# Kernel tuning notes

Measured on AMD Instinct MI355X. Metric: run time of the kernel, lower is better.

The kernel has to match this reference:

```python
import jax, jax.numpy as jnp
import numpy as np

B, N, T, F = 256, 64, 50, 2
E, H, R = 64, 128, 30


def setup_inputs() -> dict:
    key = jax.random.key(0)
    ks = jax.random.split(key, 16)
    rn = lambda k, shp, s=0.1: jax.random.normal(k, shp, jnp.float32) * s
    return {
        "src": jax.random.normal(ks[0], (B, N, T, F), jnp.float32),
        "trg": jax.random.normal(ks[1], (B, R, F), jnp.float32),
        # spatial encoder: residual Linear (no bias) + GCNConv weight/bias
        "W_res": rn(ks[2], (F, E)),
        "W_gcn": rn(ks[3], (F, E)),
        "b_gcn": jnp.zeros((E,), jnp.float32),
        # encoder LSTMCell (PyTorch gate order i,f,g,o); b = b_ih + b_hh fused
        "W_ih_e": rn(ks[4], (E, 4 * H)),
        "W_hh_e": rn(ks[5], (H, 4 * H)),
        "b_e": jnp.zeros((4 * H,), jnp.float32),
        # decoder: linear1 (2->E), LSTMCell (E->H), linear2 (H->2)
        "W1": rn(ks[6], (F, E)),
        "b1": jnp.zeros((E,), jnp.float32),
        "W_ih_d": rn(ks[7], (E, 4 * H)),
        "W_hh_d": rn(ks[8], (H, 4 * H)),
        "b_d": jnp.zeros((4 * H,), jnp.float32),
        "W2": rn(ks[9], (H, F)),
        "b2": jnp.zeros((F,), jnp.float32),
    }


def _lstm_step(h, c, xt, W_ih, W_hh, b):
    g = xt @ W_ih + h @ W_hh + b
    i, f, gg, o = jnp.split(g, 4, axis=-1)
    c = jax.nn.sigmoid(f) * c + jax.nn.sigmoid(i) * jnp.tanh(gg)
    h = jax.nn.sigmoid(o) * jnp.tanh(c)
    return h, c


def _forward(src, trg, W_res, W_gcn, b_gcn, W_ih_e, W_hh_e, b_e,
             W1, b1, W_ih_d, W_hh_d, b_d, W2, b2):
    # ---- EncoderSpatial: distance-weighted GCNConv over per-(sample,t) full graph ----
    x = jnp.swapaxes(src, 1, 2)                       # [B,T,N,F]
    diff = x[:, :, :, None, :] - x[:, :, None, :, :]  # [B,T,N,N,F]
    dist = jnp.linalg.norm(diff, axis=-1)             # [B,T,N,N]
    dist = jnp.where(dist == 0.0, 1e-6, dist)
    w = jnp.minimum(1.0 / dist, 1.0)                  # clipped inverse distance
    eye = jnp.eye(N, dtype=x.dtype)
    w = w * (1.0 - eye) + eye                         # remove self loops, GCN adds them with weight 1
    dinv = jnp.sum(w, axis=-1) ** -0.5                # [B,T,N]
    A = w * dinv[..., :, None] * dinv[..., None, :]   # sym-normalized adjacency
    gcn = jnp.einsum('btij,btjf->btif', A, x @ W_gcn) + b_gcn
    enc = jax.nn.relu(gcn + x @ W_res)                # [B,T,N,E]
    emb = enc[:, :, 0, :]                             # target-agent embeddings [B,T,E]
    inputs0 = x[:, :, 0, :]                           # target-agent positions  [B,T,F]

    # ---- LSTM encoder over T steps ----
    def enc_step(carry, xt):
        h, c = _lstm_step(carry[0], carry[1], xt, W_ih_e, W_hh_e, b_e)
        return (h, c), None
    h0 = jnp.zeros((B, H), src.dtype)
    (h, c), _ = jax.lax.scan(enc_step, (h0, h0), jnp.swapaxes(emb, 0, 1))

    def dec_step(carry, _):
        xin, h, c = carry
        ed = jax.nn.relu(xin @ W1 + b1)
        h, c = _lstm_step(h, c, ed, W_ih_d, W_hh_d, b_d)
        out = h @ W2 + b2
        return (out, h, c), out
    (_, _, _), outs = jax.lax.scan(dec_step, (inputs0[:, -1, :], h, c), None, length=R)
    return jnp.swapaxes(outs, 0, 1)                   # reg: [B,R,F]


def reference(src, trg, W_res, W_gcn, b_gcn, W_ih_e, W_hh_e, b_e,
              W1, b1, W_ih_d, W_hh_d, b_d, W2, b2):
    return _forward(src, trg, W_res, W_gcn, b_gcn, W_ih_e, W_hh_e, b_e,
                    W1, b1, W_ih_d, W_hh_d, b_d, W2, b2)
```

## Files before the change

### kernel.cpp

```cpp
#include <hip/hip_runtime.h>

#define Bn 256
#define Nn 64
#define Tn 50
#define Fn 2
#define En 64
#define Hn 128
#define Rn 30
#define G4 512

typedef _Float16 h2    __attribute__((ext_vector_type(2)));
typedef _Float16 f16x8 __attribute__((ext_vector_type(8)));
typedef float    f32x4 __attribute__((ext_vector_type(4)));

__device__ __forceinline__ float sigf(float x) {
    return __builtin_amdgcn_rcpf(1.0f + __expf(-x));
}
__device__ __forceinline__ float tanh_fast(float x) {
    return 1.0f - 2.0f * __builtin_amdgcn_rcpf(__expf(2.0f * x) + 1.0f);
}
__device__ __forceinline__ float dot2(h2 a, h2 b, float c) {
#if __has_builtin(__builtin_amdgcn_fdot2)
    return __builtin_amdgcn_fdot2(a, b, c, false);
#else
    return fmaf((float)a[0], (float)b[0], fmaf((float)a[1], (float)b[1], c));
#endif
}
__device__ __forceinline__ h2 pack2(float a, float b) {
    h2 r; r[0] = (_Float16)a; r[1] = (_Float16)b; return r;
}
__device__ __forceinline__ h2 bch2(float u)        { return __builtin_bit_cast(h2, u); }
__device__ __forceinline__ h2 bchu(unsigned int u) { return __builtin_bit_cast(h2, u); }

__device__ __forceinline__ void blockbar() {
    __builtin_amdgcn_sched_barrier(0);
    asm volatile("s_waitcnt lgkmcnt(0)" ::: "memory");
    __builtin_amdgcn_s_barrier();
    __builtin_amdgcn_sched_barrier(0);
}

__global__ __launch_bounds__(512) void k_pre(const float* __restrict__ src,
                                             const float* __restrict__ W_res,
                                             const float* __restrict__ W_gcn,
                                             const float* __restrict__ b_gcn,
                                             const float* __restrict__ W_ih_e,
                                             const float* __restrict__ b_e,
                                             _Float16* __restrict__ XI)
{
    const int tid  = threadIdx.x;
    const int lane = tid & 63;
    const int wv   = tid >> 6;
    const int task0 = blockIdx.x * 16;

    __shared__ __align__(16) _Float16 elds[16][64];
    __shared__ float2 xs[8][Nn];

    const float wg0 = W_gcn[lane], wg1 = W_gcn[En + lane];
    const float wr0 = W_res[lane], wr1 = W_res[En + lane];
    const float bg  = b_gcn[lane];

    #pragma unroll
    for (int it = 0; it < 2; it++) {
        const int task = task0 + (wv << 1) + it;
        const int b = task / Tn;
        const int t = task - b * Tn;

        const float2 xv = *reinterpret_cast<const float2*>(
            src + (((size_t)b * Nn + lane) * Tn + t) * Fn);
        const float x0 = xv.x, x1 = xv.y;
        xs[wv][lane] = xv;

        float rowsum = 0.0f, w0 = 0.0f;
        #pragma unroll
        for (int k = 0; k < Nn; k++) {
            const float2 o = xs[wv][k];
            const float dx = x0 - o.x, dy = x1 - o.y;
            const float w = fminf(__builtin_amdgcn_rsqf(dx * dx + dy * dy), 1.0f);
            rowsum += w;
            if (k == 0) w0 = w;
        }
        const float dinv  = __builtin_amdgcn_rsqf(rowsum);
        const float dinv0 = __shfl(dinv, 0);
        const float a = w0 * dinv0 * dinv;

        float p0 = a * x0, p1 = a * x1;
        #pragma unroll
        for (int off = 32; off; off >>= 1) {
            p0 += __shfl_xor(p0, off);
            p1 += __shfl_xor(p1, off);
        }
        const float xa = __shfl(x0, 0);
        const float xb = __shfl(x1, 0);

        const float v = p0 * wg0 + p1 * wg1 + bg + xa * wr0 + xb * wr1;
        elds[(wv << 1) + it][lane] = (_Float16)fmaxf(v, 0.0f);
    }

    const int colp = (tid & 3) * 128 + (tid >> 2);
    h2 wih[32];
    #pragma unroll
    for (int q = 0; q < 32; q++)
        wih[q] = pack2(W_ih_e[(size_t)(2 * q) * G4 + colp],
                       W_ih_e[(size_t)(2 * q + 1) * G4 + colp]);
    const float be = b_e[colp];
    __syncthreads();

    #pragma unroll
    for (int it = 0; it < 16; it++) {
        const float4* e4 = reinterpret_cast<const float4*>(&elds[it][0]);
        float acc = be;
        #pragma unroll
        for (int q = 0; q < 8; q++) {
            const float4 u = e4[q];
            acc = dot2(wih[4 * q + 0], bch2(u.x), acc);
            acc = dot2(wih[4 * q + 1], bch2(u.y), acc);
            acc = dot2(wih[4 * q + 2], bch2(u.z), acc);
            acc = dot2(wih[4 * q + 3], bch2(u.w), acc);
        }
        XI[(size_t)(task0 + it) * G4 + tid] = (_Float16)acc;
    }
}

__global__ __launch_bounds__(512) void k_seq(
    const _Float16* __restrict__ XI,
    const float* __restrict__ src,
    const float* __restrict__ W_hh_e,
    const float* __restrict__ W1,     const float* __restrict__ b1,
    const float* __restrict__ W_ih_d, const float* __restrict__ W_hh_d,
    const float* __restrict__ b_d,
    const float* __restrict__ W2,     const float* __restrict__ b2,
    float* __restrict__ out)
{
    const int tid  = threadIdx.x;
    const int lane = tid & 63;
    const int wv   = tid >> 6;
    const int l15  = lane & 15;
    const int lg   = lane >> 4;
    const int cc   = wv * 16 + l15;
    const int bq0  = blockIdx.x * 4;

    __shared__ __align__(16) _Float16 hbuf[2][576];
    __shared__ __align__(16) _Float16 wi_frag[8 * 8 * 64 * 8];
    __shared__ __align__(16) float    redw[2][8][4][2];

    f16x8 bfr[4][4];
    #pragma unroll
    for (int g = 0; g < 4; g++)
        #pragma unroll
        for (int kt = 0; kt < 4; kt++) {
            f16x8 v;
            #pragma unroll
            for (int j = 0; j < 8; j++)
                v[j] = (_Float16)W_hh_e[(size_t)(kt * 32 + lg * 8 + j) * G4 + g * 128 + cc];
            bfr[g][kt] = v;
        }

    if (tid < 288) reinterpret_cast<float*>(&hbuf[0][0])[tid] = 0.0f;

    float cst = 0.0f;
    char* const hb0 = reinterpret_cast<char*>(&hbuf[0][0]);
    char* const hb1 = reinterpret_cast<char*>(&hbuf[1][0]);
    const _Float16* const XIrow = XI + (size_t)(bq0 + lg) * Tn * G4 + cc * 4;

    uint2 xi0, xi1;
    xi0 = *reinterpret_cast<const uint2*>(XIrow + 0 * G4);
    xi1 = *reinterpret_cast<const uint2*>(XIrow + 1 * G4);
    __syncthreads();

    for (int t = 0; t < Tn; t += 2) {
        uint2 nxt0, nxt1;
        const int t2 = (t + 2 < Tn) ? t + 2 : t;
        const int t3 = (t + 3 < Tn) ? t + 3 : t;
        nxt0 = *reinterpret_cast<const uint2*>(XIrow + (size_t)t2 * G4);
        nxt1 = *reinterpret_cast<const uint2*>(XIrow + (size_t)t3 * G4);

        #pragma unroll
        for (int half = 0; half < 2; half++) {
            char* const hr = half ? hb1 : hb0;
            char* const hw = half ? hb0 : hb1;
            const uint2 xiv = half ? xi1 : xi0;

            f16x8 af[4];
            #pragma unroll
            for (int kt = 0; kt < 4; kt++)
                af[kt] = *reinterpret_cast<const f16x8*>(
                    hr + (l15 & 3) * 288 + kt * 64 + lg * 16);

            f32x4 acc[4] = {};
            #pragma unroll
            for (int kt = 0; kt < 4; kt++)
                #pragma unroll
                for (int g = 0; g < 4; g++)
                    acc[g] = __builtin_amdgcn_mfma_f32_16x16x32_f16(af[kt], bfr[g][kt], acc[g], 0, 0, 0);

            float ga[4];
            #pragma unroll
            for (int g = 0; g < 4; g++) {
                const float s01 = (lg & 1) ? acc[g][1] : acc[g][0];
                const float s23 = (lg & 1) ? acc[g][3] : acc[g][2];
                ga[g] = (lg & 2) ? s23 : s01;
            }

            const h2 lo = bchu(xiv.x);
            const h2 hi = bchu(xiv.y);
            const float gi = ga[0] + (float)lo[0];
            const float gf = ga[1] + (float)lo[1];
            const float gg = ga[2] + (float)hi[0];
            const float go = ga[3] + (float)hi[1];
            cst = sigf(gf) * cst + sigf(gi) * tanh_fast(gg);
            const float hv = sigf(go) * tanh_fast(cst);

            *reinterpret_cast<_Float16*>(hw + lg * 288 + cc * 2) = (_Float16)hv;
            blockbar();
        }
        xi0 = nxt0; xi1 = nxt1;
    }

    #pragma unroll
    for (int g = 0; g < 4; g++)
        #pragma unroll
        for (int kt = 0; kt < 4; kt++) {
            f16x8 v;
            #pragma unroll
            for (int j = 0; j < 8; j++)
                v[j] = (_Float16)W_hh_d[(size_t)(kt * 32 + lg * 8 + j) * G4 + g * 128 + cc];
            bfr[g][kt] = v;
        }
    #pragma unroll
    for (int g = 0; g < 4; g++)
        #pragma unroll
        for (int kt2 = 0; kt2 < 2; kt2++) {
            f16x8 v;
            #pragma unroll
            for (int j = 0; j < 8; j++)
                v[j] = (_Float16)W_ih_d[(size_t)(kt2 * 32 + lg * 8 + j) * G4 + g * 128 + cc];
            *reinterpret_cast<f16x8*>(&wi_frag[((wv * 8 + g * 2 + kt2) * 64 + lane) * 8]) = v;
        }

    const float bd0 = b_d[cc], bd1 = b_d[128 + cc], bd2 = b_d[256 + cc], bd3 = b_d[384 + cc];
    const float w2a = W2[cc * 2], w2b = W2[cc * 2 + 1];
    const float b20 = b2[0], b21 = b2[1];
    const int   mb  = l15 & 3;

    h2 w1ah[8], w1bh[8], b1h[8];
    #pragma unroll
    for (int q = 0; q < 8; q++) {
        const int e0 = (q >> 2) * 32 + lg * 8 + (q & 3) * 2;
        w1ah[q] = pack2(W1[e0],      W1[e0 + 1]);
        w1bh[q] = pack2(W1[En + e0], W1[En + e0 + 1]);
        b1h[q]  = pack2(b1[e0],      b1[e0 + 1]);
    }

    float o0 = src[((size_t)(bq0 + mb) * Nn * Tn + (Tn - 1)) * Fn + 0];
    float o1 = src[((size_t)(bq0 + mb) * Nn * Tn + (Tn - 1)) * Fn + 1];
    __syncthreads();

    for (int r = 0; r < Rn; r++) {
        const int cur = r & 1;
        char* const hr = cur ? hb1 : hb0;
        char* const hw = cur ? hb0 : hb1;

        const h2 o0h = pack2(o0, o0);
        const h2 o1h = pack2(o1, o1);
        f16x8 ae[2];
        #pragma unroll
        for (int kt2 = 0; kt2 < 2; kt2++)
            #pragma unroll
            for (int p = 0; p < 4; p++) {
                h2 v = w1ah[kt2 * 4 + p] * o0h + w1bh[kt2 * 4 + p] * o1h + b1h[kt2 * 4 + p];
                v[0] = v[0] > (_Float16)0 ? v[0] : (_Float16)0;
                v[1] = v[1] > (_Float16)0 ? v[1] : (_Float16)0;
                ae[kt2][2 * p]     = v[0];
                ae[kt2][2 * p + 1] = v[1];
            }

        f16x8 af[4];
        #pragma unroll
        for (int kt = 0; kt < 4; kt++)
            af[kt] = *reinterpret_cast<const f16x8*>(
                hr + (l15 & 3) * 288 + kt * 64 + lg * 16);

        f32x4 acc[4] = {};
        #pragma unroll
        for (int kt = 0; kt < 4; kt++)
            #pragma unroll
            for (int g = 0; g < 4; g++)
                acc[g] = __builtin_amdgcn_mfma_f32_16x16x32_f16(af[kt], bfr[g][kt], acc[g], 0, 0, 0);
        #pragma unroll
        for (int g = 0; g < 4; g++)
            #pragma unroll
            for (int kt2 = 0; kt2 < 2; kt2++) {
                const f16x8 bfe = *reinterpret_cast<const f16x8*>(
                    &wi_frag[((wv * 8 + g * 2 + kt2) * 64 + lane) * 8]);
                acc[g] = __builtin_amdgcn_mfma_f32_16x16x32_f16(ae[kt2], bfe, acc[g], 0, 0, 0);
            }

        float ga[4];
        #pragma unroll
        for (int g = 0; g < 4; g++) {
            const float s01 = (lg & 1) ? acc[g][1] : acc[g][0];
            const float s23 = (lg & 1) ? acc[g][3] : acc[g][2];
            ga[g] = (lg & 2) ? s23 : s01;
        }

        const float gi = ga[0] + bd0;
        const float gf = ga[1] + bd1;
        const float gg = ga[2] + bd2;
        const float go = ga[3] + bd3;
        cst = sigf(gf) * cst + sigf(gi) * tanh_fast(gg);
        const float hv = sigf(go) * tanh_fast(cst);
        *reinterpret_cast<_Float16*>(hw + lg * 288 + cc * 2) = (_Float16)hv;

        float p0 = hv * w2a, p1 = hv * w2b;
        #pragma unroll
        for (int off = 1; off < 16; off <<= 1) {
            p0 += __shfl_xor(p0, off);
            p1 += __shfl_xor(p1, off);
        }
        if (l15 == 0) {
            redw[cur][wv][lg][0] = p0;
            redw[cur][wv][lg][1] = p1;
        }
        blockbar();

        o0 = b20; o1 = b21;
        #pragma unroll
        for (int w8 = 0; w8 < 8; w8++) {
            const float2 rr = *reinterpret_cast<const float2*>(&redw[cur][w8][mb][0]);
            o0 += rr.x; o1 += rr.y;
        }
        if (wv == 4 && l15 < 2) {
            float oo = l15 ? b21 : b20;
            #pragma unroll
            for (int w8 = 0; w8 < 8; w8++) oo += redw[cur][w8][lg][l15];
            out[(((size_t)(bq0 + lg)) * Rn + r) * Fn + l15] = oo;
        }
    }
}

extern "C" void kernel_launch(void* const* d_in, const int* in_sizes, int n_in,
                              void* d_out, int out_size, void* d_ws, size_t ws_size,
                              hipStream_t stream)
{
    const float* src    = (const float*)d_in[0];
    const float* W_res  = (const float*)d_in[2];
    const float* W_gcn  = (const float*)d_in[3];
    const float* b_gcn  = (const float*)d_in[4];
    const float* W_ih_e = (const float*)d_in[5];
    const float* W_hh_e = (const float*)d_in[6];
    const float* b_e    = (const float*)d_in[7];
    const float* W1     = (const float*)d_in[8];
    const float* b1     = (const float*)d_in[9];
    const float* W_ih_d = (const float*)d_in[10];
    const float* W_hh_d = (const float*)d_in[11];
    const float* b_d    = (const float*)d_in[12];
    const float* W2     = (const float*)d_in[13];
    const float* b2     = (const float*)d_in[14];

    float* out = (float*)d_out;
    _Float16* XI = (_Float16*)d_ws;

    k_pre<<<(Bn * Tn) / 16, 512, 0, stream>>>(src, W_res, W_gcn, b_gcn, W_ih_e, b_e, XI);
    k_seq<<<Bn / 4, 512, 0, stream>>>(XI, src,
                                      W_hh_e,
                                      W1, b1,
                                      W_ih_d, W_hh_d, b_d,
                                      W2, b2, out);
}
```

Before: 104.8 us.

## Fuse encoder input projection into sequential LSTM kernel via MFMA on staged embeddings

```diff
diff --git a/kernel.cpp b/kernel.cpp
--- a/kernel.cpp
+++ b/kernel.cpp
@@ -8,6 +8,7 @@
 #define Hn 128
 #define Rn 30
 #define G4 512
+#define EMS 6416
 
 typedef _Float16 h2    __attribute__((ext_vector_type(2)));
 typedef _Float16 f16x8 __attribute__((ext_vector_type(8)));
@@ -19,18 +20,9 @@
 __device__ __forceinline__ float tanh_fast(float x) {
     return 1.0f - 2.0f * __builtin_amdgcn_rcpf(__expf(2.0f * x) + 1.0f);
 }
-__device__ __forceinline__ float dot2(h2 a, h2 b, float c) {
-#if __has_builtin(__builtin_amdgcn_fdot2)
-    return __builtin_amdgcn_fdot2(a, b, c, false);
-#else
-    return fmaf((float)a[0], (float)b[0], fmaf((float)a[1], (float)b[1], c));
-#endif
-}
 __device__ __forceinline__ h2 pack2(float a, float b) {
     h2 r; r[0] = (_Float16)a; r[1] = (_Float16)b; return r;
 }
-__device__ __forceinline__ h2 bch2(float u)        { return __builtin_bit_cast(h2, u); }
-__device__ __forceinline__ h2 bchu(unsigned int u) { return __builtin_bit_cast(h2, u); }
 
 __device__ __forceinline__ void blockbar() {
     __builtin_amdgcn_sched_barrier(0);
@@ -39,92 +31,57 @@
     __builtin_amdgcn_sched_barrier(0);
 }
 
-__global__ __launch_bounds__(512) void k_pre(const float* __restrict__ src,
+__global__ __launch_bounds__(512) void k_emb(const float* __restrict__ src,
                                              const float* __restrict__ W_res,
                                              const float* __restrict__ W_gcn,
                                              const float* __restrict__ b_gcn,
-                                             const float* __restrict__ W_ih_e,
-                                             const float* __restrict__ b_e,
-                                             _Float16* __restrict__ XI)
+                                             _Float16* __restrict__ emb)
 {
-    const int tid  = threadIdx.x;
-    const int lane = tid & 63;
-    const int wv   = tid >> 6;
-    const int task0 = blockIdx.x * 16;
-
-    __shared__ __align__(16) _Float16 elds[16][64];
+    const int lane = threadIdx.x & 63;
+    const int wv   = threadIdx.x >> 6;
+    const int task = blockIdx.x * 8 + wv;
+    const int b = task / Tn;
+    const int t = task - b * Tn;
+
     __shared__ float2 xs[8][Nn];
 
-    const float wg0 = W_gcn[lane], wg1 = W_gcn[En + lane];
-    const float wr0 = W_res[lane], wr1 = W_res[En + lane];
-    const float bg  = b_gcn[lane];
-
-    #pragma unroll
-    for (int it = 0; it < 2; it++) {
-        const int task = task0 + (wv << 1) + it;
-        const int b = task / Tn;
-        const int t = task - b * Tn;
-
-        const float2 xv = *reinterpret_cast<const float2*>(
-            src + (((size_t)b * Nn + lane) * Tn + t) * Fn);
-        const float x0 = xv.x, x1 = xv.y;
-        xs[wv][lane] = xv;
-
-        float rowsum = 0.0f, w0 = 0.0f;
-        #pragma unroll
-        for (int k = 0; k < Nn; k++) {
-            const float2 o = xs[wv][k];
-            const float dx = x0 - o.x, dy = x1 - o.y;
-            const float w = fminf(__builtin_amdgcn_rsqf(dx * dx + dy * dy), 1.0f);
-            rowsum += w;
-            if (k == 0) w0 = w;
-        }
-        const float dinv  = __builtin_amdgcn_rsqf(rowsum);
-        const float dinv0 = __shfl(dinv, 0);
-        const float a = w0 * dinv0 * dinv;
-
-        float p0 = a * x0, p1 = a * x1;
-        #pragma unroll
-        for (int off = 32; off; off >>= 1) {
-            p0 += __shfl_xor(p0, off);
-            p1 += __shfl_xor(p1, off);
-        }
-        const float xa = __shfl(x0, 0);
-        const float xb = __shfl(x1, 0);
-
-        const float v = p0 * wg0 + p1 * wg1 + bg + xa * wr0 + xb * wr1;
-        elds[(wv << 1) + it][lane] = (_Float16)fmaxf(v, 0.0f);
-    }
-
-    const int colp = (tid & 3) * 128 + (tid >> 2);
-    h2 wih[32];
-    #pragma unroll
-    for (int q = 0; q < 32; q++)
-        wih[q] = pack2(W_ih_e[(size_t)(2 * q) * G4 + colp],
-                       W_ih_e[(size_t)(2 * q + 1) * G4 + colp]);
-    const float be = b_e[colp];
-    __syncthreads();
-
-    #pragma unroll
-    for (int it = 0; it < 16; it++) {
-        const float4* e4 = reinterpret_cast<const float4*>(&elds[it][0]);
-        float acc = be;
-        #pragma unroll
-        for (int q = 0; q < 8; q++) {
-            const float4 u = e4[q];
-            acc = dot2(wih[4 * q + 0], bch2(u.x), acc);
-            acc = dot2(wih[4 * q + 1], bch2(u.y), acc);
-            acc = dot2(wih[4 * q + 2], bch2(u.z), acc);
-            acc = dot2(wih[4 * q + 3], bch2(u.w), acc);
-        }
-        XI[(size_t)(task0 + it) * G4 + tid] = (_Float16)acc;
-    }
+    const float2 xv = *reinterpret_cast<const float2*>(
+        src + (((size_t)b * Nn + lane) * Tn + t) * Fn);
+    const float x0 = xv.x, x1 = xv.y;
+    xs[wv][lane] = xv;
+
+    float rowsum = 0.0f, w0 = 0.0f;
+    #pragma unroll
+    for (int k = 0; k < Nn; k++) {
+        const float2 o = xs[wv][k];
+        const float dx = x0 - o.x, dy = x1 - o.y;
+        const float w = fminf(__builtin_amdgcn_rsqf(dx * dx + dy * dy), 1.0f);
+        rowsum += w;
+        if (k == 0) w0 = w;
+    }
+    const float dinv  = __builtin_amdgcn_rsqf(rowsum);
+    const float dinv0 = __shfl(dinv, 0);
+    const float a = w0 * dinv0 * dinv;
+
+    float p0 = a * x0, p1 = a * x1;
+    #pragma unroll
+    for (int off = 32; off; off >>= 1) {
+        p0 += __shfl_xor(p0, off);
+        p1 += __shfl_xor(p1, off);
+    }
+    const float xa = __shfl(x0, 0);
+    const float xb = __shfl(x1, 0);
+
+    const float v = p0 * W_gcn[lane] + p1 * W_gcn[En + lane] + b_gcn[lane]
+                  + xa * W_res[lane] + xb * W_res[En + lane];
+    emb[(size_t)task * En + lane] = (_Float16)fmaxf(v, 0.0f);
 }
 
 __global__ __launch_bounds__(512) void k_seq(
-    const _Float16* __restrict__ XI,
+    const _Float16* __restrict__ emb,
     const float* __restrict__ src,
-    const float* __restrict__ W_hh_e,
+    const float* __restrict__ W_hh_e, const float* __restrict__ W_ih_e,
+    const float* __restrict__ b_e,
     const float* __restrict__ W1,     const float* __restrict__ b1,
     const float* __restrict__ W_ih_d, const float* __restrict__ W_hh_d,
     const float* __restrict__ b_d,
@@ -138,10 +95,14 @@
     const int lg   = lane >> 4;
     const int cc   = wv * 16 + l15;
     const int bq0  = blockIdx.x * 4;
+    const int mb   = l15 & 3;
 
     __shared__ __align__(16) _Float16 hbuf[2][576];
     __shared__ __align__(16) _Float16 wi_frag[8 * 8 * 64 * 8];
+    __shared__ __align__(16) _Float16 emb_lds[4 * 3208];
     __shared__ __align__(16) float    redw[2][8][4][2];
+
+    char* const embbase = reinterpret_cast<char*>(&emb_lds[0]);
 
     f16x8 bfr[4][4];
     #pragma unroll
@@ -155,65 +116,84 @@
             bfr[g][kt] = v;
         }
 
+    #pragma unroll
+    for (int g = 0; g < 4; g++)
+        #pragma unroll
+        for (int kt2 = 0; kt2 < 2; kt2++) {
+            f16x8 v;
+            #pragma unroll
+            for (int j = 0; j < 8; j++)
+                v[j] = (_Float16)W_ih_e[(size_t)(kt2 * 32 + lg * 8 + j) * G4 + g * 128 + cc];
+            *reinterpret_cast<f16x8*>(&wi_frag[((wv * 8 + g * 2 + kt2) * 64 + lane) * 8]) = v;
+        }
+
+    {
+        const _Float16* eg = emb + (size_t)bq0 * Tn * En;
+        for (int i = tid; i < 1600; i += 512) {
+            const int m = i / 400;
+            const int r = i - m * 400;
+            const uint4 v = *reinterpret_cast<const uint4*>(eg + i * 8);
+            *reinterpret_cast<uint4*>(embbase + m * EMS + r * 16) = v;
+        }
+    }
+
     if (tid < 288) reinterpret_cast<float*>(&hbuf[0][0])[tid] = 0.0f;
+
+    const float be0 = b_e[cc], be1 = b_e[128 + cc], be2 = b_e[256 + cc], be3 = b_e[384 + cc];
 
     float cst = 0.0f;
     char* const hb0 = reinterpret_cast<char*>(&hbuf[0][0]);
     char* const hb1 = reinterpret_cast<char*>(&hbuf[1][0]);
-    const _Float16* const XIrow = XI + (size_t)(bq0 + lg) * Tn * G4 + cc * 4;
-
-    uint2 xi0, xi1;
-    xi0 = *reinterpret_cast<const uint2*>(XIrow + 0 * G4);
-    xi1 = *reinterpret_cast<const uint2*>(XIrow + 1 * G4);
     __syncthreads();
 
-    for (int t = 0; t < Tn; t += 2) {
-        uint2 nxt0, nxt1;
-        const int t2 = (t + 2 < Tn) ? t + 2 : t;
-        const int t3 = (t + 3 < Tn) ? t + 3 : t;
-        nxt0 = *reinterpret_cast<const uint2*>(XIrow + (size_t)t2 * G4);
-        nxt1 = *reinterpret_cast<const uint2*>(XIrow + (size_t)t3 * G4);
-
-        #pragma unroll
-        for (int half = 0; half < 2; half++) {
-            char* const hr = half ? hb1 : hb0;
-            char* const hw = half ? hb0 : hb1;
-            const uint2 xiv = half ? xi1 : xi0;
-
-            f16x8 af[4];
-            #pragma unroll
-            for (int kt = 0; kt < 4; kt++)
-                af[kt] = *reinterpret_cast<const f16x8*>(
-                    hr + (l15 & 3) * 288 + kt * 64 + lg * 16);
-
-            f32x4 acc[4] = {};
-            #pragma unroll
-            for (int kt = 0; kt < 4; kt++)
-                #pragma unroll
-                for (int g = 0; g < 4; g++)
-                    acc[g] = __builtin_amdgcn_mfma_f32_16x16x32_f16(af[kt], bfr[g][kt], acc[g], 0, 0, 0);
-
-            float ga[4];
-            #pragma unroll
-            for (int g = 0; g < 4; g++) {
-                const float s01 = (lg & 1) ? acc[g][1] : acc[g][0];
-                const float s23 = (lg & 1) ? acc[g][3] : acc[g][2];
-                ga[g] = (lg & 2) ? s23 : s01;
+    for (int t = 0; t < Tn; t++) {
+        const int cur = t & 1;
+        char* const hr = cur ? hb1 : hb0;
+        char* const hw = cur ? hb0 : hb1;
+
+        f16x8 af[4];
+        #pragma unroll
+        for (int kt = 0; kt < 4; kt++)
+            af[kt] = *reinterpret_cast<const f16x8*>(
+                hr + (l15 & 3) * 288 + kt * 64 + lg * 16);
+        f16x8 ae[2];
+        #pragma unroll
+        for (int kt2 = 0; kt2 < 2; kt2++)
+            ae[kt2] = *reinterpret_cast<const f16x8*>(
+                embbase + mb * EMS + t * 128 + kt2 * 64 + lg * 16);
+
+        f32x4 acc[4] = {};
+        #pragma unroll
+        for (int kt = 0; kt < 4; kt++)
+            #pragma unroll
+            for (int g = 0; g < 4; g++)
+                acc[g] = __builtin_amdgcn_mfma_f32_16x16x32_f16(af[kt], bfr[g][kt], acc[g], 0, 0, 0);
+        #pragma unroll
+        for (int g = 0; g < 4; g++)
+            #pragma unroll
+            for (int kt2 = 0; kt2 < 2; kt2++) {
+                const f16x8 bfe = *reinterpret_cast<const f16x8*>(
+                    &wi_frag[((wv * 8 + g * 2 + kt2) * 64 + lane) * 8]);
+                acc[g] = __builtin_amdgcn_mfma_f32_16x16x32_f16(ae[kt2], bfe, acc[g], 0, 0, 0);
             }
 
-            const h2 lo = bchu(xiv.x);
-            const h2 hi = bchu(xiv.y);
-            const float gi = ga[0] + (float)lo[0];
-            const float gf = ga[1] + (float)lo[1];
-            const float gg = ga[2] + (float)hi[0];
-            const float go = ga[3] + (float)hi[1];
-            cst = sigf(gf) * cst + sigf(gi) * tanh_fast(gg);
-            const float hv = sigf(go) * tanh_fast(cst);
-
-            *reinterpret_cast<_Float16*>(hw + lg * 288 + cc * 2) = (_Float16)hv;
-            blockbar();
-        }
-        xi0 = nxt0; xi1 = nxt1;
+        float ga[4];
+        #pragma unroll
+        for (int g = 0; g < 4; g++) {
+            const float s01 = (lg & 1) ? acc[g][1] : acc[g][0];
+            const float s23 = (lg & 1) ? acc[g][3] : acc[g][2];
+            ga[g] = (lg & 2) ? s23 : s01;
+        }
+
+        const float gi = ga[0] + be0;
+        const float gf = ga[1] + be1;
+        const float gg = ga[2] + be2;
+        const float go = ga[3] + be3;
+        cst = sigf(gf) * cst + sigf(gi) * tanh_fast(gg);
+        const float hv = sigf(go) * tanh_fast(cst);
+
+        *reinterpret_cast<_Float16*>(hw + lg * 288 + cc * 2) = (_Float16)hv;
+        blockbar();
     }
 
     #pragma unroll
@@ -240,7 +220,6 @@
     const float bd0 = b_d[cc], bd1 = b_d[128 + cc], bd2 = b_d[256 + cc], bd3 = b_d[384 + cc];
     const float w2a = W2[cc * 2], w2b = W2[cc * 2 + 1];
     const float b20 = b2[0], b21 = b2[1];
-    const int   mb  = l15 & 3;
 
     h2 w1ah[8], w1bh[8], b1h[8];
     #pragma unroll
@@ -358,11 +337,11 @@
     const float* b2     = (const float*)d_in[14];
 
     float* out = (float*)d_out;
-    _Float16* XI = (_Float16*)d_ws;
-
-    k_pre<<<(Bn * Tn) / 16, 512, 0, stream>>>(src, W_res, W_gcn, b_gcn, W_ih_e, b_e, XI);
-    k_seq<<<Bn / 4, 512, 0, stream>>>(XI, src,
-                                      W_hh_e,
+    _Float16* emb = (_Float16*)d_ws;
+
+    k_emb<<<(Bn * Tn) / 8, 512, 0, stream>>>(src, W_res, W_gcn, b_gcn, emb);
+    k_seq<<<Bn / 4, 512, 0, stream>>>(emb, src,
+                                      W_hh_e, W_ih_e, b_e,
                                       W1, b1,
                                       W_ih_d, W_hh_d, b_d,
                                       W2, b2, out);
```

After: 90.44 us. 1.16x faster.
